# Optimization experiments

Measured on AMD Instinct MI355X. Metric: run time of the kernel, lower is better.

## Reference

```python
import jax, jax.numpy as jnp
import numpy as np

N_NODES = 50000
N_EDGES = 1600000
FEAT = 1536
HID = 200
NCLS = 2


def setup_inputs() -> dict:
    key = jax.random.key(0)
    ks = jax.random.split(key, 12)
    x = jax.random.normal(ks[0], (N_NODES, FEAT), dtype=jnp.float32)
    edge_src = jax.random.randint(ks[1], (N_EDGES,), 0, N_NODES, dtype=jnp.int32)
    edge_dst = jax.random.randint(ks[2], (N_EDGES,), 0, N_NODES, dtype=jnp.int32)
    edge_w = jax.random.uniform(ks[3], (N_EDGES,), dtype=jnp.float32)
    s1 = 1.0 / np.sqrt(768.0)
    s2 = 1.0 / np.sqrt(HID)
    return {
        "x": x,
        "edge_src": edge_src,
        "edge_dst": edge_dst,
        "edge_w": edge_w,
        "W1a": jax.random.normal(ks[4], (768, HID), dtype=jnp.float32) * s1,
        "b1a": jnp.zeros((HID,), jnp.float32),
        "W2a": jax.random.normal(ks[5], (HID, NCLS), dtype=jnp.float32) * s2,
        "b2a": jnp.zeros((NCLS,), jnp.float32),
        "W1b": jax.random.normal(ks[6], (768, HID), dtype=jnp.float32) * s1,
        "b1b": jnp.zeros((HID,), jnp.float32),
        "W2b": jax.random.normal(ks[7], (HID, NCLS), dtype=jnp.float32) * s2,
        "b2b": jnp.zeros((NCLS,), jnp.float32),
    }


def _gcn_conv(x, W, b, src, dst, w, activation):
    # GCNConv: activation(A @ (X @ W) + b) with sparse A given as edge list
    h = x @ W                                  # [N, out] dense transform first (out < in)
    msg = h[src] * w[:, None]                  # [E, out] weighted messages
    agg = jax.ops.segment_sum(msg, dst, num_segments=x.shape[0])  # [N, out]
    return activation(agg + b)


def reference(x, edge_src, edge_dst, edge_w, W1a, b1a, W2a, b2a, W1b, b1b, W2b, b2b):
    x1 = x[:, :768]
    x2 = x[:, 768:]
    # Expert 1 branch (dropout is identity at inference)
    h1 = _gcn_conv(x1, W1a, b1a, edge_src, edge_dst, edge_w, jax.nn.relu)
    p1 = _gcn_conv(h1, W2a, b2a, edge_src, edge_dst, edge_w,
                   lambda z: jax.nn.softmax(z, axis=-1))
    # Expert 2 branch
    h2 = _gcn_conv(x2, W1b, b1b, edge_src, edge_dst, edge_w, jax.nn.relu)
    p2 = _gcn_conv(h2, W2b, b2b, edge_src, edge_dst, edge_w,
                   lambda z: jax.nn.softmax(z, axis=-1))
    # Inference-mode soft voting: elementwise max then renormalize
    votes = jnp.maximum(p1, p2)
    votes = votes / jnp.sum(votes, axis=1, keepdims=True)
    return votes
```

## Files before the change

### kernel.cpp

```cpp
#include <hip/hip_runtime.h>
#include <hip/hip_fp16.h>

#define N_NODES 50000
#define N_EDGES 1600000
#define FEAT    1536
#define HID     200
#define HIDP    208
#define HPW     400
#define KDIM    768
#define CAP     96
#define KSTEPS  24

typedef _Float16 half8 __attribute__((ext_vector_type(8)));
typedef _Float16 half4 __attribute__((ext_vector_type(4)));
typedef float   float4v __attribute__((ext_vector_type(4)));

__global__ void prep_kernel(const float* __restrict__ W1a, const float* __restrict__ b1a,
                            const float* __restrict__ W2a,
                            const float* __restrict__ W1b, const float* __restrict__ b1b,
                            const float* __restrict__ W2b,
                            _Float16* __restrict__ Wht, float* __restrict__ b1comb,
                            float* __restrict__ W2comb) {
  int i = blockIdx.x * 256 + threadIdx.x;
  if (i < 2 * HIDP * KDIM) {
    int br = i / (HIDP * KDIM);
    int r  = i % (HIDP * KDIM);
    int n = r / KDIM, k = r % KDIM;
    const float* W = br ? W1b : W1a;
    Wht[i] = (n < HID) ? (_Float16)W[k * HID + n] : (_Float16)0.0f;
  }
  if (i < 2 * HID) {
    int br = i / HID, cc = i % HID;
    const float* b  = br ? b1b : b1a;
    const float* W2 = br ? W2b : W2a;
    b1comb[i]       = b[cc];
    W2comb[2*i + 0] = W2[cc*2 + 0];
    W2comb[2*i + 1] = W2[cc*2 + 1];
  }
}

__global__ void append_kernel(const int* __restrict__ src, const int* __restrict__ dst,
                              const float* __restrict__ w, int* __restrict__ cnt,
                              int2* __restrict__ ssw) {
  int i = blockIdx.x * 256 + threadIdx.x;
  if (i < N_EDGES) {
    int d = dst[i];
    int pos = atomicAdd(&cnt[d], 1);
    if (pos < CAP)
      ssw[(size_t)d * CAP + pos] = make_int2(src[i], __float_as_int(w[i]));
  }
}

__global__ __launch_bounds__(256, 2) void gemm1_kernel(const float* __restrict__ x,
    const _Float16* __restrict__ Wht, _Float16* __restrict__ hpre) {
  const int m0 = blockIdx.x * 128;
  const int br = blockIdx.y;
  const int tid = threadIdx.x;
  const int wave = tid >> 6, lane = tid & 63;
  __shared__ _Float16 Alds[2][128][40];
  __shared__ _Float16 Blds[2][HIDP][40];
  const _Float16* Wb = Wht + (size_t)br * HIDP * KDIM;
  float4v acc[2][13];
#pragma unroll
  for (int mt = 0; mt < 2; ++mt)
#pragma unroll
    for (int nt = 0; nt < 13; ++nt) acc[mt][nt] = (float4v){0.f, 0.f, 0.f, 0.f};

  const int mlo = lane & 15, kq = (lane >> 4) * 8;

  const float* aptr[4];
#pragma unroll
  for (int p = 0; p < 4; ++p) {
    int idx = tid + p * 256;
    int row = idx >> 3, c4 = idx & 7;
    int grow = m0 + row; if (grow > N_NODES - 1) grow = N_NODES - 1;
    aptr[p] = x + (size_t)grow * FEAT + br * KDIM + c4 * 4;
  }
  const _Float16* bptr[4];
  bool bok[4];
#pragma unroll
  for (int q = 0; q < 4; ++q) {
    int idx = tid + q * 256;
    bok[q] = (idx < HIDP * 4);
    int n = bok[q] ? (idx >> 2) : 0, c = bok[q] ? (idx & 3) : 0;
    bptr[q] = Wb + n * KDIM + c * 8;
  }

  float4v apre[4];
  half8  bpre[4];
#pragma unroll
  for (int p = 0; p < 4; ++p) apre[p] = __builtin_nontemporal_load((const float4v*)aptr[p]);
#pragma unroll
  for (int q = 0; q < 4; ++q) bpre[q] = *(const half8*)bptr[q];

  for (int t = 0; t < KSTEPS; ++t) {
    const int cur = t & 1;
#pragma unroll
    for (int p = 0; p < 4; ++p) {
      int idx = tid + p * 256;
      int row = idx >> 3, c4 = idx & 7;
      half4 hv = {(_Float16)apre[p][0], (_Float16)apre[p][1],
                  (_Float16)apre[p][2], (_Float16)apre[p][3]};
      *(half4*)&Alds[cur][row][c4 * 4] = hv;
    }
#pragma unroll
    for (int q = 0; q < 4; ++q) {
      int idx = tid + q * 256;
      int n = idx >> 2, c = idx & 3;
      if (bok[q]) *(half8*)&Blds[cur][n][c * 8] = bpre[q];
    }
    if (t < KSTEPS - 1) {
      const int k1 = (t + 1) * 32;
#pragma unroll
      for (int p = 0; p < 4; ++p)
        apre[p] = __builtin_nontemporal_load((const float4v*)(aptr[p] + k1));
#pragma unroll
      for (int q = 0; q < 4; ++q) bpre[q] = *(const half8*)(bptr[q] + k1);
    }
    __syncthreads();
    half8 a0 = *(half8*)&Alds[cur][wave * 32 + mlo][kq];
    half8 a1 = *(half8*)&Alds[cur][wave * 32 + 16 + mlo][kq];
#pragma unroll
    for (int nt = 0; nt < 13; ++nt) {
      half8 b = *(half8*)&Blds[cur][nt * 16 + mlo][kq];
      acc[0][nt] = __builtin_amdgcn_mfma_f32_16x16x32_f16(a0, b, acc[0][nt], 0, 0, 0);
      acc[1][nt] = __builtin_amdgcn_mfma_f32_16x16x32_f16(a1, b, acc[1][nt], 0, 0, 0);
    }
  }
  const int nlo = lane & 15, mq = (lane >> 4) * 4;
#pragma unroll
  for (int mt = 0; mt < 2; ++mt)
#pragma unroll
    for (int nt = 0; nt < 13; ++nt) {
      int c = nt * 16 + nlo;
      if (c < HID)
#pragma unroll
        for (int r = 0; r < 4; ++r) {
          int row = m0 + wave * 32 + mt * 16 + mq + r;
          if (row < N_NODES)
            hpre[(size_t)row * HPW + br * HID + c] = (_Float16)acc[mt][nt][r];
        }
    }
}

__global__ __launch_bounds__(256) void agg1_kernel(const int2* __restrict__ ssw,
    const int* __restrict__ cnt, const _Float16* __restrict__ hpre,
    const float* __restrict__ b1comb, const float* __restrict__ W2comb,
    float4v* __restrict__ qtab) {
  const int d = blockIdx.x * 4 + (threadIdx.x >> 6);
  const int lane = threadIdx.x & 63;
  const bool actA = (lane < 25);
  const bool actB = (lane >= 32 && lane < 57);
  const bool act  = actA || actB;
  const int col = actA ? lane * 8 : (actB ? HID + (lane - 32) * 8 : 0);
  const int e0 = d * CAP;
  const int deg = min(cnt[d], CAP);
  const int e1 = e0 + deg;
  float acc[8];
#pragma unroll
  for (int j = 0; j < 8; ++j) acc[j] = 0.f;
  if (act) {
    const _Float16* hp = hpre + col;
    int e = e0;
    for (; e + 3 < e1; e += 4) {
      int2 s0 = ssw[e], s1 = ssw[e + 1], s2 = ssw[e + 2], s3 = ssw[e + 3];
      half8 h0 = *(const half8*)(hp + (size_t)s0.x * HPW);
      half8 h1 = *(const half8*)(hp + (size_t)s1.x * HPW);
      half8 h2 = *(const half8*)(hp + (size_t)s2.x * HPW);
      half8 h3 = *(const half8*)(hp + (size_t)s3.x * HPW);
      float w0 = __int_as_float(s0.y), w1 = __int_as_float(s1.y);
      float w2 = __int_as_float(s2.y), w3 = __int_as_float(s3.y);
#pragma unroll
      for (int j = 0; j < 8; ++j)
        acc[j] += w0 * (float)h0[j] + w1 * (float)h1[j]
                + w2 * (float)h2[j] + w3 * (float)h3[j];
    }
    for (; e < e1; ++e) {
      int2 s0 = ssw[e];
      half8 h0 = *(const half8*)(hp + (size_t)s0.x * HPW);
      float w0 = __int_as_float(s0.y);
#pragma unroll
      for (int j = 0; j < 8; ++j) acc[j] += w0 * (float)h0[j];
    }
  }
  float p0 = 0.f, p1 = 0.f;
  if (act) {
#pragma unroll
    for (int j = 0; j < 8; ++j) {
      int c = col + j;
      float h = fmaxf(acc[j] + b1comb[c], 0.f);
      p0 += h * W2comb[2 * c + 0];
      p1 += h * W2comb[2 * c + 1];
    }
  }
#pragma unroll
  for (int off = 16; off > 0; off >>= 1) {
    p0 += __shfl_xor(p0, off);
    p1 += __shfl_xor(p1, off);
  }
  float q2 = __shfl(p0, 32);
  float q3 = __shfl(p1, 32);
  if (lane == 0) qtab[d] = (float4v){p0, p1, q2, q3};
}

__global__ __launch_bounds__(256) void agg2_kernel(const int2* __restrict__ ssw,
    const int* __restrict__ cnt, const float4v* __restrict__ qtab,
    const float* __restrict__ b2a, const float* __restrict__ b2b,
    float* __restrict__ out) {
  const int d = blockIdx.x * 8 + (threadIdx.x >> 5);
  const int lane = threadIdx.x & 31;
  const int e0 = d * CAP;
  const int e1 = e0 + min(cnt[d], CAP);
  float a0 = 0.f, a1 = 0.f, a2 = 0.f, a3 = 0.f;
  for (int e = e0 + lane; e < e1; e += 32) {
    int2 sw = ssw[e];
    float w = __int_as_float(sw.y);
    float4v q = qtab[sw.x];
    a0 += w * q[0]; a1 += w * q[1]; a2 += w * q[2]; a3 += w * q[3];
  }
#pragma unroll
  for (int off = 16; off > 0; off >>= 1) {
    a0 += __shfl_xor(a0, off);
    a1 += __shfl_xor(a1, off);
    a2 += __shfl_xor(a2, off);
    a3 += __shfl_xor(a3, off);
  }
  if (lane == 0) {
    float za0 = a0 + b2a[0], za1 = a1 + b2a[1];
    float zb0 = a2 + b2b[0], zb1 = a3 + b2b[1];
    float m1 = fmaxf(za0, za1);
    float ea0 = __expf(za0 - m1), ea1 = __expf(za1 - m1);
    float p10 = ea0 / (ea0 + ea1), p11 = ea1 / (ea0 + ea1);
    float m2 = fmaxf(zb0, zb1);
    float eb0 = __expf(zb0 - m2), eb1 = __expf(zb1 - m2);
    float p20 = eb0 / (eb0 + eb1), p21 = eb1 / (eb0 + eb1);
    float v0 = fmaxf(p10, p20), v1 = fmaxf(p11, p21);
    float s = v0 + v1;
    out[d * 2 + 0] = v0 / s;
    out[d * 2 + 1] = v1 / s;
  }
}

extern "C" void kernel_launch(void* const* d_in, const int* in_sizes, int n_in,
                              void* d_out, int out_size, void* d_ws, size_t ws_size,
                              hipStream_t stream) {
  const float* x        = (const float*)d_in[0];
  const int*   edge_src = (const int*)d_in[1];
  const int*   edge_dst = (const int*)d_in[2];
  const float* edge_w   = (const float*)d_in[3];
  const float* W1a = (const float*)d_in[4];
  const float* b1a = (const float*)d_in[5];
  const float* W2a = (const float*)d_in[6];
  const float* b2a = (const float*)d_in[7];
  const float* W1b = (const float*)d_in[8];
  const float* b1b = (const float*)d_in[9];
  const float* W2b = (const float*)d_in[10];
  const float* b2b = (const float*)d_in[11];
  float* out = (float*)d_out;

  char* ws = (char*)d_ws;
  size_t off = 0;
  auto alloc = [&](size_t bytes) -> void* {
    void* p = ws + off;
    off = (off + bytes + 255) & ~(size_t)255;
    return p;
  };
  _Float16* Wht  = (_Float16*)alloc((size_t)2 * HIDP * KDIM * sizeof(_Float16));
  float* b1comb  = (float*)alloc(2 * HID * sizeof(float));
  float* W2comb  = (float*)alloc(2 * HID * 2 * sizeof(float));
  int* cnt       = (int*)alloc(N_NODES * sizeof(int));
  int2* ssw      = (int2*)alloc((size_t)N_NODES * CAP * sizeof(int2));
  float4v* qtab  = (float4v*)alloc((size_t)N_NODES * sizeof(float4v));
  _Float16* hpre = (_Float16*)alloc((size_t)N_NODES * HPW * sizeof(_Float16));
  (void)ws_size; (void)in_sizes; (void)n_in; (void)out_size;

  (void)hipMemsetAsync(cnt, 0, N_NODES * sizeof(int), stream);

  prep_kernel<<<dim3((2 * HIDP * KDIM + 255) / 256), dim3(256), 0, stream>>>(
      W1a, b1a, W2a, W1b, b1b, W2b, Wht, b1comb, W2comb);
  append_kernel<<<dim3((N_EDGES + 255) / 256), dim3(256), 0, stream>>>(
      edge_src, edge_dst, edge_w, cnt, ssw);
  gemm1_kernel<<<dim3((N_NODES + 127) / 128, 2), dim3(256), 0, stream>>>(x, Wht, hpre);
  agg1_kernel<<<dim3(N_NODES / 4), dim3(256), 0, stream>>>(ssw, cnt, hpre, b1comb, W2comb, qtab);
  agg2_kernel<<<dim3(N_NODES / 8), dim3(256), 0, stream>>>(ssw, cnt, qtab, b2a, b2b, out);
}
```

Baseline: 749.2 us.

## Fuse edge bucketing into GEMM launch and fold counter reset into prep

Merges the edge-append (bucketing by destination) kernel into the GEMM kernel as a horizontal fusion. Every fourth block, up to 256 of them, runs a grid-stride append loop, and the rest compute GEMM tiles. The count reset moves from a memset into prep_kernel. The aim is to overlap the atomic-heavy, latency-bound append with the compute-bound GEMM and to cut two launches. The risk is that append blocks hold the GEMM's large LDS allocation and occupancy, and that the block-to-tile remapping adds some complexity.

```diff
diff --git a/kernel.cpp b/kernel.cpp
--- a/kernel.cpp
+++ b/kernel.cpp
@@ -10,6 +10,8 @@
 #define KDIM    768
 #define CAP     96
 #define KSTEPS  24
+#define NAPP    256
+#define NGEMM   782
 
 typedef _Float16 half8 __attribute__((ext_vector_type(8)));
 typedef _Float16 half4 __attribute__((ext_vector_type(4)));
@@ -20,7 +22,7 @@
                             const float* __restrict__ W1b, const float* __restrict__ b1b,
                             const float* __restrict__ W2b,
                             _Float16* __restrict__ Wht, float* __restrict__ b1comb,
-                            float* __restrict__ W2comb) {
+                            float* __restrict__ W2comb, int* __restrict__ cnt) {
   int i = blockIdx.x * 256 + threadIdx.x;
   if (i < 2 * HIDP * KDIM) {
     int br = i / (HIDP * KDIM);
@@ -37,28 +39,35 @@
     W2comb[2*i + 0] = W2[cc*2 + 0];
     W2comb[2*i + 1] = W2[cc*2 + 1];
   }
-}
-
-__global__ void append_kernel(const int* __restrict__ src, const int* __restrict__ dst,
-                              const float* __restrict__ w, int* __restrict__ cnt,
-                              int2* __restrict__ ssw) {
-  int i = blockIdx.x * 256 + threadIdx.x;
-  if (i < N_EDGES) {
-    int d = dst[i];
-    int pos = atomicAdd(&cnt[d], 1);
-    if (pos < CAP)
-      ssw[(size_t)d * CAP + pos] = make_int2(src[i], __float_as_int(w[i]));
-  }
-}
-
-__global__ __launch_bounds__(256, 2) void gemm1_kernel(const float* __restrict__ x,
-    const _Float16* __restrict__ Wht, _Float16* __restrict__ hpre) {
-  const int m0 = blockIdx.x * 128;
-  const int br = blockIdx.y;
-  const int tid = threadIdx.x;
-  const int wave = tid >> 6, lane = tid & 63;
+  if (i < N_NODES) cnt[i] = 0;
+}
+
+__global__ __launch_bounds__(256, 2) void fusedAG_kernel(
+    const int* __restrict__ esrc, const int* __restrict__ edst,
+    const float* __restrict__ ew, int* __restrict__ cnt, int2* __restrict__ ssw,
+    const float* __restrict__ x, const _Float16* __restrict__ Wht,
+    _Float16* __restrict__ hpre) {
   __shared__ _Float16 Alds[2][128][40];
   __shared__ _Float16 Blds[2][HIDP][40];
+  const int bid = blockIdx.x;
+  const int tid = threadIdx.x;
+
+  const bool is_app = ((bid & 3) == 3) && ((bid >> 2) < NAPP);
+  if (is_app) {
+    const int k = bid >> 2;
+    for (int i = k * 256 + tid; i < N_EDGES; i += NAPP * 256) {
+      int d = edst[i];
+      int pos = atomicAdd(&cnt[d], 1);
+      if (pos < CAP)
+        ssw[(size_t)d * CAP + pos] = make_int2(esrc[i], __float_as_int(ew[i]));
+    }
+    return;
+  }
+  const int napp_before = min(NAPP, (bid + 1) >> 2);
+  const int gid = bid - napp_before;
+  const int m0 = (gid >> 1) * 128;
+  const int br = gid & 1;
+  const int wave = tid >> 6, lane = tid & 63;
   const _Float16* Wb = Wht + (size_t)br * HIDP * KDIM;
   float4v acc[2][13];
 #pragma unroll
@@ -274,13 +283,12 @@
   _Float16* hpre = (_Float16*)alloc((size_t)N_NODES * HPW * sizeof(_Float16));
   (void)ws_size; (void)in_sizes; (void)n_in; (void)out_size;
 
-  (void)hipMemsetAsync(cnt, 0, N_NODES * sizeof(int), stream);
-
   prep_kernel<<<dim3((2 * HIDP * KDIM + 255) / 256), dim3(256), 0, stream>>>(
-      W1a, b1a, W2a, W1b, b1b, W2b, Wht, b1comb, W2comb);
-  append_kernel<<<dim3((N_EDGES + 255) / 256), dim3(256), 0, stream>>>(
-      edge_src, edge_dst, edge_w, cnt, ssw);
-  gemm1_kernel<<<dim3((N_NODES + 127) / 128, 2), dim3(256), 0, stream>>>(x, Wht, hpre);
-  agg1_kernel<<<dim3(N_NODES / 4), dim3(256), 0, stream>>>(ssw, cnt, hpre, b1comb, W2comb, qtab);
-  agg2_kernel<<<dim3(N_NODES / 8), dim3(256), 0, stream>>>(ssw, cnt, qtab, b2a, b2b, out);
-}
+      W1a, b1a, W2a, W1b, b1b, W2b, Wht, b1comb, W2comb, cnt);
+  fusedAG_kernel<<<dim3(NGEMM + NAPP), dim3(256), 0, stream>>>(
+      edge_src, edge_dst, edge_w, cnt, ssw, x, Wht, hpre);
+  agg1_kernel<<<dim3(N_NODES / 4), dim3(256), 0, stream>>>(
+      ssw, cnt, hpre, b1comb, W2comb, qtab);
+  agg2_kernel<<<dim3(N_NODES / 8), dim3(256), 0, stream>>>(
+      ssw, cnt, qtab, b2a, b2b, out);
+}
```

Result: faster. 702.6 us (-6.2%).
